# Performance work log

Measured on AMD Instinct MI355X. Metric: run time of the kernel, lower is better.

## Reference

```python
import jax, jax.numpy as jnp
import numpy as np

S, W, H = 1025, 128, 200


def setup_inputs() -> dict:
    key = jax.random.key(0)
    ks = jax.random.split(key, 40)
    n = lambda k, shape, s=1.0: jax.random.normal(k, shape, dtype=jnp.float32) * s
    p = {}
    p["words"] = n(ks[0], (S, W, H))
    p["lengths"] = jax.random.randint(ks[1], (S,), 1, W + 1, dtype=jnp.int32)
    p["h0w"] = n(ks[2], (S, H))
    p["c0w"] = n(ks[3], (S, H))
    p["h0p"] = n(ks[4], (H,))
    p["c0p"] = n(ks[5], (H,))
    p["h0q"] = n(ks[6], (H,))
    p["c0q"] = n(ks[7], (H,))
    ki = 8
    for nm in ("ctx", "tgt", "prev", "post"):
        p[f"wih_{nm}"] = n(ks[ki], (4 * H, H), 0.05); ki += 1
        p[f"whh_{nm}"] = n(ks[ki], (4 * H, H), 0.05); ki += 1
        p[f"bih_{nm}"] = n(ks[ki], (4 * H,), 0.05); ki += 1
        p[f"bhh_{nm}"] = n(ks[ki], (4 * H,), 0.05); ki += 1
    p["fc_w"] = n(ks[ki], (H, 2 * H), 0.05); ki += 1
    p["fc_b"] = n(ks[ki], (H,), 0.05)
    return p


def _lstm_seq(x, h0, c0, wih, whh, bih, bhh):
    """x: [T,H]; returns outputs [T,H]. Torch LSTM gate order: i,f,g,o."""
    gx = x @ wih.T + (bih + bhh)  # precompute input projection: [T,4H]
    def step(carry, g):
        h, c = carry
        gates = g + h @ whh.T
        i, f, gg, o = jnp.split(gates, 4, axis=-1)
        c = jax.nn.sigmoid(f) * c + jax.nn.sigmoid(i) * jnp.tanh(gg)
        h = jax.nn.sigmoid(o) * jnp.tanh(c)
        return (h, c), h
    _, hs = jax.lax.scan(step, (h0, c0), gx)
    return hs


def reference(words, lengths, h0w, c0w, h0p, c0p, h0q, c0q,
              wih_ctx, whh_ctx, bih_ctx, bhh_ctx,
              wih_tgt, whh_tgt, bih_tgt, bhh_tgt,
              wih_prev, whh_prev, bih_prev, bhh_prev,
              wih_post, whh_post, bih_post, bhh_post,
              fc_w, fc_b):
    Sn = words.shape[0]
    mid = (Sn - 1) // 2
    # Word-level context RNN over all sentences (batched scan)
    ctx_outs = jax.vmap(_lstm_seq, in_axes=(0, 0, 0, None, None, None, None))(
        words, h0w, c0w, wih_ctx, whh_ctx, bih_ctx, bhh_ctx)  # [S,W,H]
    # sentence embedding = output at last real word (ragged lengths)
    emb = ctx_outs[jnp.arange(Sn), lengths - 1]  # [S,H]
    # middle sentence uses target RNN instead
    tgt_outs = _lstm_seq(words[mid], h0w[mid], c0w[mid], wih_tgt, whh_tgt, bih_tgt, bhh_tgt)
    emb = emb.at[mid].set(tgt_outs[lengths[mid] - 1])
    # prev RNN over sentences 0..mid; keep output at mid
    prev_hs = _lstm_seq(emb[:mid + 1], h0p, c0p, wih_prev, whh_prev, bih_prev, bhh_prev)
    prev_out = prev_hs[-1]
    # post RNN over sentences S-1..mid (reversed); keep output at mid
    post_hs = _lstm_seq(emb[mid:][::-1], h0q, c0q, wih_post, whh_post, bih_post, bhh_post)
    post_out = post_hs[-1]
    feat = jnp.concatenate([prev_out, post_out])  # [2H]
    return feat @ fc_w.T + fc_b  # [H]
```

## Files before the change

kernel.cpp:

```cpp
#include <hip/hip_runtime.h>
#include <cmath>

typedef unsigned short u16;
typedef short bf16x8 __attribute__((ext_vector_type(8)));
typedef float f32x4 __attribute__((ext_vector_type(4)));

#define S_N 1025
#define W_N 128
#define H_N 200
#define FH_N 800
#define KP 232
#define SGP 911
#define SGW 804
#define MID 512
#define NT 56
#define PKT (NT * 7 * 512)
#define PKC 544
#define QKS 136
#define FRAGSZ (7 * PKC)

__device__ __forceinline__ float bf2f(u16 u) {
  unsigned int x = ((unsigned int)u) << 16;
  return __builtin_bit_cast(float, x);
}
__device__ __forceinline__ u16 f2bf(float f) {
  unsigned int x = __builtin_bit_cast(unsigned int, f);
  x += 0x7fffu + ((x >> 16) & 1u);
  return (u16)(x >> 16);
}
#define LOG2E 1.44269504088896f
__device__ __forceinline__ float fsigm(float x) {
  float e = __builtin_amdgcn_exp2f(-fabsf(x) * LOG2E);
  float p = __builtin_amdgcn_rcpf(1.f + e);
  return x >= 0.f ? p : 1.f - p;
}
__device__ __forceinline__ float ftanh(float x) {
  float e = __builtin_amdgcn_exp2f(-2.f * fabsf(x) * LOG2E);
  float th = (1.f - e) * __builtin_amdgcn_rcpf(1.f + e);
  return x >= 0.f ? th : -th;
}

__device__ __forceinline__ const bf16x8* pkptr(const u16* pk, int tt, int kcc, int lane) {
  return (const bf16x8*)(pk + (size_t)((tt * 7 + kcc) * 512 + lane * 8));
}
__device__ __forceinline__ int fidx(int m, int k) {
  return (k >> 5) * PKC + ((k >> 3) & 3) * QKS + m * 8 + (k & 7);
}
__device__ __forceinline__ const bf16x8* frg(const u16* base, int kcc, int lane) {
  return (const bf16x8*)(base + kcc * PKC + (lane >> 4) * QKS + (lane & 15) * 8);
}

__global__ __launch_bounds__(256) void k_w2b(
    const float* __restrict__ p0, const float* __restrict__ p1,
    const float* __restrict__ p2, const float* __restrict__ p3,
    const float* __restrict__ p4, const float* __restrict__ p5,
    const float* __restrict__ p6, const float* __restrict__ p7,
    u16* __restrict__ dst)
{
  int i = blockIdx.x * 256 + threadIdx.x;
  if (i >= 8 * PKT) return;
  int w = i / PKT, r = i - w * PKT;
  int tt = r / 3584;
  int q = r - tt * 3584;
  int kcc = q >> 9;
  int lane = (q >> 3) & 63;
  int j = q & 7;
  int col = lane & 15, quad = lane >> 4;
  int gate = tt * 16 + col;
  int k = kcc * 32 + quad * 8 + j;
  const float* ps[8] = {p0, p1, p2, p3, p4, p5, p6, p7};
  u16 v = 0;
  if (gate < FH_N && k < H_N) v = f2bf(ps[w][(size_t)gate * H_N + k]);
  dst[i] = v;
}

__global__ __launch_bounds__(1024) void k_sort(
    const int* __restrict__ lengths, int* __restrict__ order)
{
  __shared__ int key[2048], val[2048];
  int tid = threadIdx.x;
  for (int v = 0; v < 2; ++v) {
    int i = tid + v * 1024;
    key[i] = (i < S_N) ? lengths[i] : -1;
    val[i] = (i < S_N) ? i : (S_N - 1);
  }
  __syncthreads();
  for (int k = 2; k <= 2048; k <<= 1)
    for (int j = k >> 1; j > 0; j >>= 1) {
      for (int v = 0; v < 2; ++v) {
        int i = tid + v * 1024;
        int ix = i ^ j;
        if (ix > i) {
          bool descRegion = ((i & k) == 0);
          int ki = key[i], kx = key[ix];
          if ((ki < kx) == descRegion) {
            key[i] = kx; key[ix] = ki;
            int tv = val[i]; val[i] = val[ix]; val[ix] = tv;
          }
        }
      }
      __syncthreads();
    }
  for (int v = 0; v < 2; ++v) {
    int i = tid + v * 1024;
    if (i < S_N) order[i] = val[i];
  }
}

__global__ __launch_bounds__(512, 1) void k_xpack(
    int c, int CH,
    const float* __restrict__ words, const int* __restrict__ lengths,
    const u16* __restrict__ wihb_ctx, const float* __restrict__ bih_ctx, const float* __restrict__ bhh_ctx,
    const u16* __restrict__ wihb_tgt, const float* __restrict__ bih_tgt, const float* __restrict__ bhh_tgt,
    float* __restrict__ gxc)
{
  const int slot = blockIdx.x % 1026;
  const int tile = blockIdx.x / 1026;
  const int t0f = tile * 16;
  const bool tg = (slot == 1025);
  const int s = tg ? MID : slot;
  const int len = lengths[s];
  const int tbase = c * CH + t0f;
  if (t0f >= CH || tbase >= len) return;
  const u16* wih = tg ? wihb_tgt : wihb_ctx;
  const float* bih = tg ? bih_tgt : bih_ctx;
  const float* bhh = tg ? bhh_tgt : bhh_ctx;

  __shared__ __align__(16) u16 sXh[FRAGSZ];
  __shared__ __align__(16) u16 sXl[FRAGSZ];
  __shared__ float sBias[FH_N];
  const int tid = threadIdx.x;
  for (int e = tid; e < FRAGSZ; e += 512) { sXh[e] = 0; sXl[e] = 0; }
  for (int e = tid; e < FH_N; e += 512) sBias[e] = bih[e] + bhh[e];
  __syncthreads();
  const int nrow = min(16, min(CH - t0f, len - tbase));
  for (int e = tid; e < nrow * H_N; e += 512) {
    int tr = e / H_N, k = e - tr * H_N;
    float v = words[((size_t)s * W_N + tbase + tr) * H_N + k];
    u16 vh = f2bf(v);
    int idx = fidx(tr, k);
    sXh[idx] = vh;
    sXl[idx] = f2bf(v - bf2f(vh));
  }
  __syncthreads();

  const int lane = tid & 63, wv = tid >> 6, quad = lane >> 4, col = lane & 15;
  const int tcg = t0f + col;
  const bool okcol = (tcg < CH) && (c * CH + tcg < len);

#pragma unroll
  for (int i = 0; i < 7; ++i) {
    int tt = wv + 8 * i;
    if (tt < 50) {
      f32x4 acc = {0.f, 0.f, 0.f, 0.f};
#pragma unroll
      for (int kcc = 0; kcc < 7; ++kcc) {
        bf16x8 Aw = *pkptr(wih, tt, kcc, lane);
        bf16x8 bxh = *frg(sXh, kcc, lane);
        bf16x8 bxl = *frg(sXl, kcc, lane);
        acc = __builtin_amdgcn_mfma_f32_16x16x32_bf16(Aw, bxh, acc, 0, 0, 0);
        acc = __builtin_amdgcn_mfma_f32_16x16x32_bf16(Aw, bxl, acc, 0, 0, 0);
      }
      if (okcol) {
        float b0 = sBias[tt * 16 + quad * 4 + 0];
        float b1 = sBias[tt * 16 + quad * 4 + 1];
        float b2 = sBias[tt * 16 + quad * 4 + 2];
        float b3 = sBias[tt * 16 + quad * 4 + 3];
        f32x4 o = {acc[0] + b0, acc[1] + b1, acc[2] + b2, acc[3] + b3};
        *(f32x4*)(gxc + ((size_t)slot * CH + tcg) * FH_N + tt * 16 + quad * 4) = o;
      }
    }
  }
}

__global__ __launch_bounds__(512, 1) void k_wrec(
    int c, int CH,
    const int* __restrict__ lengths, const int* __restrict__ order,
    const float* __restrict__ h0w, const float* __restrict__ c0w,
    const u16* __restrict__ whhb_ctx, const u16* __restrict__ whhb_tgt,
    const float* __restrict__ gxc,
    float* __restrict__ stateH, float* __restrict__ stateC,
    float* __restrict__ emb)
{
  const int tid = threadIdx.x;
  const int b = blockIdx.x;
  const bool is_tgt = (b == 65);
  const u16* whh = is_tgt ? whhb_tgt : whhb_ctx;

  __shared__ __align__(16) u16 sBh[FRAGSZ];
  __shared__ __align__(16) u16 sBl[FRAGSZ];
  __shared__ float sG[16 * SGW];
  __shared__ int sLen[16], sId[16];

  if (tid < 16) {
    int slot = b * 16 + tid;
    int s = is_tgt ? MID : order[min(slot, S_N - 1)];
    sId[tid] = s;
    sLen[tid] = lengths[s];
  }
  __syncthreads();
  int Lmax = 1;
  for (int m = 0; m < 16; ++m) Lmax = max(Lmax, sLen[m]);
  if (c * CH >= Lmax) return;

  const int lane = tid & 63;
  const int wv = tid >> 6;
  const int quad = lane >> 4;
  const int col = lane & 15;

  bf16x8 afr[7][7];
#pragma unroll
  for (int i = 0; i < 7; ++i)
#pragma unroll
    for (int kcc = 0; kcc < 7; ++kcc)
      afr[i][kcc] = *pkptr(whh, wv + 8 * i, kcc, lane);

  for (int e = tid; e < FRAGSZ; e += 512) { sBh[e] = 0; sBl[e] = 0; }
  __syncthreads();

  float creg[7];
#pragma unroll
  for (int rr = 0; rr < 7; ++rr) {
    int e = tid + 512 * rr;
    if (e < 16 * H_N) {
      int m = e / H_N, j = e - m * H_N;
      float h, cc;
      if (c == 0) {
        int s = sId[m];
        h = h0w[(size_t)s * H_N + j];
        cc = c0w[(size_t)s * H_N + j];
      } else {
        h = stateH[(size_t)(b * 16 + m) * H_N + j];
        cc = stateC[(size_t)(b * 16 + m) * H_N + j];
      }
      creg[rr] = cc;
      u16 hh = f2bf(h);
      int idx = fidx(m, j);
      sBh[idx] = hh;
      sBl[idx] = f2bf(h - bf2f(hh));
    }
  }
  __syncthreads();

#pragma unroll 1
  for (int tc = 0; tc < CH; ++tc) {
    const int t = c * CH + tc;
    if (t >= Lmax) break;

    f32x4 acc[7];
#pragma unroll
    for (int i = 0; i < 7; ++i) { f32x4 z = {0.f, 0.f, 0.f, 0.f}; acc[i] = z; }
#pragma unroll
    for (int kcc = 0; kcc < 7; ++kcc) {
      bf16x8 bh = *frg(sBh, kcc, lane);
      bf16x8 bl = *frg(sBl, kcc, lane);
#pragma unroll
      for (int i = 0; i < 7; ++i) {
        if (wv + 8 * i < 50) {
          acc[i] = __builtin_amdgcn_mfma_f32_16x16x32_bf16(afr[i][kcc], bh, acc[i], 0, 0, 0);
          acc[i] = __builtin_amdgcn_mfma_f32_16x16x32_bf16(afr[i][kcc], bl, acc[i], 0, 0, 0);
        }
      }
    }
#pragma unroll
    for (int i = 0; i < 7; ++i) {
      int tt = wv + 8 * i;
      if (tt < 50)
        *(f32x4*)(sG + col * SGW + tt * 16 + quad * 4) = acc[i];
    }

    float gv[7][4];
#pragma unroll
    for (int rr = 0; rr < 7; ++rr) {
      int e = tid + 512 * rr;
      if (e < 16 * H_N) {
        int m = e / H_N, j = e - m * H_N;
        int gslot = is_tgt ? 1025 : sId[m];
        const float* gp = gxc + ((size_t)gslot * CH + tc) * FH_N + j;
        gv[rr][0] = gp[0];
        gv[rr][1] = gp[H_N];
        gv[rr][2] = gp[2 * H_N];
        gv[rr][3] = gp[3 * H_N];
      }
    }
    __syncthreads();

#pragma unroll
    for (int rr = 0; rr < 7; ++rr) {
      int e = tid + 512 * rr;
      if (e < 16 * H_N) {
        int m = e / H_N, j = e - m * H_N;
        const float* gRow = sG + m * SGW + j;
        float ig = gRow[0] + gv[rr][0];
        float fg = gRow[H_N] + gv[rr][1];
        float gg = gRow[2 * H_N] + gv[rr][2];
        float og = gRow[3 * H_N] + gv[rr][3];
        float nc = fsigm(fg) * creg[rr] + fsigm(ig) * ftanh(gg);
        float nh = fsigm(og) * ftanh(nc);
        creg[rr] = nc;
        u16 hh = f2bf(nh);
        int idx = fidx(m, j);
        sBh[idx] = hh;
        sBl[idx] = f2bf(nh - bf2f(hh));
        if (t == sLen[m] - 1) {
          int s = sId[m];
          if (is_tgt) {
            if (m == 0) emb[(size_t)MID * H_N + j] = nh;
          } else if (s != MID) {
            emb[(size_t)s * H_N + j] = nh;
          }
        }
      }
    }
    __syncthreads();
  }

#pragma unroll
  for (int rr = 0; rr < 7; ++rr) {
    int e = tid + 512 * rr;
    if (e < 16 * H_N) {
      int m = e / H_N, j = e - m * H_N;
      int idx = fidx(m, j);
      stateH[(size_t)(b * 16 + m) * H_N + j] = bf2f(sBh[idx]) + bf2f(sBl[idx]);
      stateC[(size_t)(b * 16 + m) * H_N + j] = creg[rr];
    }
  }
}

__global__ __launch_bounds__(512, 1) void k_word_s(
    const float* __restrict__ words, const int* __restrict__ lengths,
    const int* __restrict__ order,
    const float* __restrict__ h0w, const float* __restrict__ c0w,
    const u16* __restrict__ wihb_ctx, const u16* __restrict__ whhb_ctx,
    const float* __restrict__ bih_ctx, const float* __restrict__ bhh_ctx,
    const u16* __restrict__ wihb_tgt, const u16* __restrict__ whhb_tgt,
    const float* __restrict__ bih_tgt, const float* __restrict__ bhh_tgt,
    float* __restrict__ emb)
{
  const int tid = threadIdx.x;
  const int b = blockIdx.x;
  const bool is_tgt = (b == 65);
  const u16* wih = is_tgt ? wihb_tgt : wihb_ctx;
  const u16* whh = is_tgt ? whhb_tgt : whhb_ctx;
  const float* bih = is_tgt ? bih_tgt : bih_ctx;
  const float* bhh = is_tgt ? bhh_tgt : bhh_ctx;

  __shared__ __align__(16) u16 sXhi[16 * KP];
  __shared__ __align__(16) u16 sXlo[16 * KP];
  __shared__ __align__(16) u16 sHi[16 * KP];
  __shared__ __align__(16) u16 sLo[16 * KP];
  __shared__ float sG[8 * SGP];
  __shared__ float sB[4 * H_N];
  __shared__ int sLen[16], sId[16];

  for (int e = tid; e < 16 * KP; e += 512) {
    sXhi[e] = 0; sXlo[e] = 0; sHi[e] = 0; sLo[e] = 0;
  }
  if (tid < 16) {
    int slot = b * 16 + tid;
    int s = is_tgt ? MID : order[min(slot, S_N - 1)];
    sId[tid] = s;
    sLen[tid] = lengths[s];
  }
  for (int e = tid; e < 4 * H_N; e += 512) sB[e] = bih[e] + bhh[e];
  __syncthreads();

  float creg[7];
#pragma unroll
  for (int r = 0; r < 7; ++r) {
    int e = tid + 512 * r;
    if (e < 16 * H_N) {
      int m = e / H_N, j = e - m * H_N;
      int s = sId[m];
      float h = h0w[(size_t)s * H_N + j];
      u16 hh = f2bf(h);
      sHi[m * KP + j] = hh;
      sLo[m * KP + j] = f2bf(h - bf2f(hh));
      creg[r] = c0w[(size_t)s * H_N + j];
    }
  }
  __syncthreads();
  int Lmax = 1;
  for (int m = 0; m < 16; ++m) Lmax = max(Lmax, sLen[m]);

  const int lane = tid & 63;
  const int wv = tid >> 6;
  const int quad = lane >> 4;
  const int col = lane & 15;
  const int hpass = quad >> 1;

  const u16* aXh = sXhi + col * KP + quad * 8;
  const u16* aXl = sXlo + col * KP + quad * 8;
  const u16* aHh = sHi  + col * KP + quad * 8;
  const u16* aHl = sLo  + col * KP + quad * 8;

#pragma unroll 1
  for (int t = 0; t < Lmax; ++t) {
    for (int e = tid; e < 16 * H_N; e += 512) {
      int m = e / H_N, k = e - m * H_N;
      float v = words[((size_t)sId[m] * W_N + t) * H_N + k];
      u16 vh = f2bf(v);
      sXhi[m * KP + k] = vh;
      sXlo[m * KP + k] = f2bf(v - bf2f(vh));
    }
    __syncthreads();

    f32x4 acc[7];
#pragma unroll
    for (int i = 0; i < 7; ++i) { f32x4 z4 = {0.f, 0.f, 0.f, 0.f}; acc[i] = z4; }

#pragma unroll
    for (int kcc = 0; kcc < 7; ++kcc) {
      bf16x8 axh = *(const bf16x8*)(aXh + kcc * 32);
      bf16x8 axl = *(const bf16x8*)(aXl + kcc * 32);
      bf16x8 ahh = *(const bf16x8*)(aHh + kcc * 32);
      bf16x8 ahl = *(const bf16x8*)(aHl + kcc * 32);
#pragma unroll
      for (int i = 0; i < 7; ++i) {
        if (wv + 8 * i < 50) {
          bf16x8 bw = *pkptr(wih, wv + 8 * i, kcc, lane);
          bf16x8 bh = *pkptr(whh, wv + 8 * i, kcc, lane);
          acc[i] = __builtin_amdgcn_mfma_f32_16x16x32_bf16(axh, bw, acc[i], 0, 0, 0);
          acc[i] = __builtin_amdgcn_mfma_f32_16x16x32_bf16(axl, bw, acc[i], 0, 0, 0);
          acc[i] = __builtin_amdgcn_mfma_f32_16x16x32_bf16(ahh, bh, acc[i], 0, 0, 0);
          acc[i] = __builtin_amdgcn_mfma_f32_16x16x32_bf16(ahl, bh, acc[i], 0, 0, 0);
        }
      }
    }

#pragma unroll 1
    for (int h = 0; h < 2; ++h) {
      if (hpass == h) {
#pragma unroll
        for (int i = 0; i < 7; ++i) {
          int tt = wv + 8 * i;
          if (tt < 50) {
#pragma unroll
            for (int r = 0; r < 4; ++r)
              sG[((quad & 1) * 4 + r) * SGP + tt * 16 + col] = acc[i][r];
          }
        }
      }
      __syncthreads();
#pragma unroll
      for (int rr = 0; rr < 7; ++rr) {
        int e = tid + 512 * rr;
        if (e < 16 * H_N) {
          int m = e / H_N, j = e - m * H_N;
          if ((m >> 3) == h) {
            const float* gRow = sG + (m - 8 * h) * SGP;
            float ig = gRow[j] + sB[j];
            float fg = gRow[H_N + j] + sB[H_N + j];
            float gg = gRow[2 * H_N + j] + sB[2 * H_N + j];
            float og = gRow[3 * H_N + j] + sB[3 * H_N + j];
            float nc = fsigm(fg) * creg[rr] + fsigm(ig) * ftanh(gg);
            float nh = fsigm(og) * ftanh(nc);
            creg[rr] = nc;
            u16 hh = f2bf(nh);
            sHi[m * KP + j] = hh;
            sLo[m * KP + j] = f2bf(nh - bf2f(hh));
            if (t == sLen[m] - 1) {
              int s = sId[m];
              if (is_tgt) {
                if (m == 0) emb[(size_t)MID * H_N + j] = nh;
              } else if (s != MID) {
                emb[(size_t)s * H_N + j] = nh;
              }
            }
          }
        }
      }
      __syncthreads();
    }
  }
}

__global__ __launch_bounds__(512) void k_gx(
    const float* __restrict__ emb,
    const u16* __restrict__ wihb_prev, const float* __restrict__ bih_prev, const float* __restrict__ bhh_prev,
    const u16* __restrict__ wihb_post, const float* __restrict__ bih_post, const float* __restrict__ bhh_post,
    float* __restrict__ gxp, float* __restrict__ gxq)
{
  const int tid = threadIdx.x;
  const int b = blockIdx.x;
  const bool post = (b >= 33);
  const int t0 = (post ? b - 33 : b) * 16;
  const u16* wih = post ? wihb_post : wihb_prev;
  const float* bih = post ? bih_post : bih_prev;
  const float* bhh = post ? bhh_post : bhh_prev;
  float* out = post ? gxq : gxp;

  __shared__ __align__(16) u16 sEhi[16 * KP];
  __shared__ __align__(16) u16 sElo[16 * KP];
  for (int e = tid; e < 16 * KP; e += 512) { sEhi[e] = 0; sElo[e] = 0; }
  __syncthreads();
  for (int e = tid; e < 16 * H_N; e += 512) {
    int m = e / H_N, k = e - m * H_N;
    int t = t0 + m;
    if (t <= 512) {
      int src = post ? (1024 - t) : t;
      float v = emb[(size_t)src * H_N + k];
      u16 vh = f2bf(v);
      sEhi[m * KP + k] = vh;
      sElo[m * KP + k] = f2bf(v - bf2f(vh));
    }
  }
  __syncthreads();

  const int lane = tid & 63;
  const int wv = tid >> 6;
  const int quad = lane >> 4;
  const int col = lane & 15;
  const u16* aH = sEhi + col * KP + quad * 8;
  const u16* aL = sElo + col * KP + quad * 8;

#pragma unroll 1
  for (int i = 0; i < 7; ++i) {
    int tt = wv + 8 * i;
    if (tt >= 50) break;
    int gate = tt * 16 + col;
    f32x4 acc = {0.f, 0.f, 0.f, 0.f};
#pragma unroll
    for (int kcc = 0; kcc < 7; ++kcc) {
      bf16x8 Ah = *(const bf16x8*)(aH + kcc * 32);
      bf16x8 Al = *(const bf16x8*)(aL + kcc * 32);
      bf16x8 bw = *pkptr(wih, tt, kcc, lane);
      acc = __builtin_amdgcn_mfma_f32_16x16x32_bf16(Ah, bw, acc, 0, 0, 0);
      acc = __builtin_amdgcn_mfma_f32_16x16x32_bf16(Al, bw, acc, 0, 0, 0);
    }
    float bias = bih[gate] + bhh[gate];
#pragma unroll
    for (int r = 0; r < 4; ++r) {
      int t = t0 + quad * 4 + r;
      if (t <= 512) out[(size_t)t * FH_N + gate] = acc[r] + bias;
    }
  }
}

__global__ __launch_bounds__(512, 1) void k_sent(
    const u16* __restrict__ whhb_prev, const u16* __restrict__ whhb_post,
    const float* __restrict__ h0p, const float* __restrict__ c0p,
    const float* __restrict__ h0q, const float* __restrict__ c0q,
    const float* __restrict__ gxp, const float* __restrict__ gxq,
    float* __restrict__ outp, float* __restrict__ outq)
{
  const int tid = threadIdx.x;
  const bool post = (blockIdx.x != 0);
  const u16* whh = post ? whhb_post : whhb_prev;
  const float* h0 = post ? h0q : h0p;
  const float* c0 = post ? c0q : c0p;
  const float* gx = post ? gxq : gxp;
  float* outv = post ? outq : outp;

  __shared__ __align__(16) u16 sHi[224];
  __shared__ __align__(16) u16 sLo[224];
  __shared__ float sGa[FH_N];
  __shared__ float sGb[FH_N];

  const int lane = tid & 63;
  const int wv = tid >> 6;
  const int quad = lane >> 4;
  const int col = lane & 15;

  bf16x8 afr[7][7];
#pragma unroll
  for (int i = 0; i < 7; ++i)
#pragma unroll
    for (int kcc = 0; kcc < 7; ++kcc)
      afr[i][kcc] = *pkptr(whh, wv + 8 * i, kcc, lane);

  if (tid < 224) { sHi[tid] = 0; sLo[tid] = 0; }
  float c = 0.f, last_h = 0.f;
  if (tid < H_N) {
    float h = h0[tid];
    u16 hh = f2bf(h);
    sHi[tid] = hh;
    sLo[tid] = f2bf(h - bf2f(hh));
    c = c0[tid];
  }
  __syncthreads();

  const u16* hb = ((lane & 8) ? sLo : sHi) + quad * 8;
  const bool wrA = (col == 0), wrB = (col == 8);

  float gc0 = 0.f, gc1 = 0.f, gc2 = 0.f, gc3 = 0.f;
  if (tid < H_N) {
    gc0 = gx[tid]; gc1 = gx[H_N + tid]; gc2 = gx[2 * H_N + tid]; gc3 = gx[3 * H_N + tid];
  }

#pragma unroll 1
  for (int t = 0; t < 513; ++t) {
    bf16x8 bfr[7];
#pragma unroll
    for (int kcc = 0; kcc < 7; ++kcc) bfr[kcc] = *(const bf16x8*)(hb + kcc * 32);

    float gn0 = 0.f, gn1 = 0.f, gn2 = 0.f, gn3 = 0.f;
    if (t + 1 < 513 && tid < H_N) {
      const float* g = gx + (size_t)(t + 1) * FH_N;
      gn0 = g[tid]; gn1 = g[H_N + tid]; gn2 = g[2 * H_N + tid]; gn3 = g[3 * H_N + tid];
    }

#pragma unroll
    for (int i = 0; i < 7; ++i) {
      int tt = wv + 8 * i;
      if (tt < 50) {
        f32x4 acc = {0.f, 0.f, 0.f, 0.f};
#pragma unroll
        for (int kcc = 0; kcc < 7; ++kcc)
          acc = __builtin_amdgcn_mfma_f32_16x16x32_bf16(afr[i][kcc], bfr[kcc], acc, 0, 0, 0);
        if (wrA) {
#pragma unroll
          for (int r = 0; r < 4; ++r) sGa[tt * 16 + quad * 4 + r] = acc[r];
        } else if (wrB) {
#pragma unroll
          for (int r = 0; r < 4; ++r) sGb[tt * 16 + quad * 4 + r] = acc[r];
        }
      }
    }
    __syncthreads();

    if (tid < H_N) {
      float ig = sGa[tid] + sGb[tid] + gc0;
      float fg = sGa[H_N + tid] + sGb[H_N + tid] + gc1;
      float gg = sGa[2 * H_N + tid] + sGb[2 * H_N + tid] + gc2;
      float og = sGa[3 * H_N + tid] + sGb[3 * H_N + tid] + gc3;
      float nc = fsigm(fg) * c + fsigm(ig) * ftanh(gg);
      float nh = fsigm(og) * ftanh(nc);
      c = nc;
      last_h = nh;
      u16 hh = f2bf(nh);
      sHi[tid] = hh;
      sLo[tid] = f2bf(nh - bf2f(hh));
    }
    gc0 = gn0; gc1 = gn1; gc2 = gn2; gc3 = gn3;
    __syncthreads();
  }
  if (tid < H_N) outv[tid] = last_h;
}

__global__ __launch_bounds__(256) void k_fc(
    const float* __restrict__ pout, const float* __restrict__ qout,
    const float* __restrict__ fc_w, const float* __restrict__ fc_b,
    float* __restrict__ out)
{
  const int tid = threadIdx.x;
  if (tid < H_N) {
    float d = fc_b[tid];
    const float* wr = fc_w + (size_t)tid * 2 * H_N;
    for (int k = 0; k < H_N; ++k) d += pout[k] * wr[k];
    for (int k = 0; k < H_N; ++k) d += qout[k] * wr[H_N + k];
    out[tid] = d;
  }
}

extern "C" void kernel_launch(void* const* d_in, const int* in_sizes, int n_in,
                              void* d_out, int out_size, void* d_ws, size_t ws_size,
                              hipStream_t stream) {
  const float* words   = (const float*)d_in[0];
  const int*   lengths = (const int*)d_in[1];
  const float* h0w = (const float*)d_in[2];
  const float* c0w = (const float*)d_in[3];
  const float* h0p = (const float*)d_in[4];
  const float* c0p = (const float*)d_in[5];
  const float* h0q = (const float*)d_in[6];
  const float* c0q = (const float*)d_in[7];
  const float* wih_ctx = (const float*)d_in[8];
  const float* whh_ctx = (const float*)d_in[9];
  const float* bih_ctx = (const float*)d_in[10];
  const float* bhh_ctx = (const float*)d_in[11];
  const float* wih_tgt = (const float*)d_in[12];
  const float* whh_tgt = (const float*)d_in[13];
  const float* bih_tgt = (const float*)d_in[14];
  const float* bhh_tgt = (const float*)d_in[15];
  const float* wih_prev = (const float*)d_in[16];
  const float* whh_prev = (const float*)d_in[17];
  const float* bih_prev = (const float*)d_in[18];
  const float* bhh_prev = (const float*)d_in[19];
  const float* wih_post = (const float*)d_in[20];
  const float* whh_post = (const float*)d_in[21];
  const float* bih_post = (const float*)d_in[22];
  const float* bhh_post = (const float*)d_in[23];
  const float* fc_w = (const float*)d_in[24];
  const float* fc_b = (const float*)d_in[25];
  (void)in_sizes; (void)n_in; (void)out_size;

  const size_t FIXF = 1448600;
  int CH = 0;
  for (int cand = 32; cand >= 1; cand >>= 1) {
    size_t needB = ((size_t)1026 * cand * 800 + FIXF) * 4 + 1056 * 4 + (size_t)8 * PKT * 2 + 256;
    if (ws_size >= needB) { CH = cand; break; }
  }

  float* ws = (float*)d_ws;
  float *gxc, *stateH, *stateC, *emb, *gxp, *gxq, *po, *qo;
  int* order;
  u16* wb;
  if (CH > 0) {
    gxc = ws;
    stateH = gxc + (size_t)1026 * CH * 800;
    stateC = stateH + 211200;
    emb = stateC + 211200;
    gxp = emb + 205000;
    gxq = gxp + 410400;
    po = gxq + 410400;
    qo = po + 200;
    order = (int*)(qo + 200);
    wb = (u16*)(order + 1056);
  } else {
    gxc = nullptr; stateH = nullptr; stateC = nullptr;
    emb = ws;
    gxp = ws + 205000;
    gxq = ws + 615400;
    po = ws + 1025800;
    qo = ws + 1026000;
    order = (int*)(ws + 1026200);
    wb = (u16*)(ws + 1027232);
  }
  u16* wihb_ctx  = wb;
  u16* whhb_ctx  = wb + PKT;
  u16* wihb_tgt  = wb + 2 * PKT;
  u16* whhb_tgt  = wb + 3 * PKT;
  u16* whhb_prev = wb + 4 * PKT;
  u16* whhb_post = wb + 5 * PKT;
  u16* wihb_prev = wb + 6 * PKT;
  u16* wihb_post = wb + 7 * PKT;

  k_w2b<<<(8 * PKT + 255) / 256, 256, 0, stream>>>(
      wih_ctx, whh_ctx, wih_tgt, whh_tgt, whh_prev, whh_post,
      wih_prev, wih_post, wb);
  k_sort<<<1, 1024, 0, stream>>>(lengths, order);

  if (CH > 0) {
    const int TT = (CH + 15) / 16;
    const int NC = (W_N + CH - 1) / CH;
    for (int c = 0; c < NC; ++c) {
      k_xpack<<<1026 * TT, 512, 0, stream>>>(c, CH, words, lengths,
                                             wihb_ctx, bih_ctx, bhh_ctx,
                                             wihb_tgt, bih_tgt, bhh_tgt, gxc);
      k_wrec<<<66, 512, 0, stream>>>(c, CH, lengths, order, h0w, c0w,
                                     whhb_ctx, whhb_tgt, gxc, stateH, stateC, emb);
    }
  } else {
    k_word_s<<<66, 512, 0, stream>>>(words, lengths, order, h0w, c0w,
                                     wihb_ctx, whhb_ctx, bih_ctx, bhh_ctx,
                                     wihb_tgt, whhb_tgt, bih_tgt, bhh_tgt, emb);
  }
  k_gx<<<66, 512, 0, stream>>>(emb, wihb_prev, bih_prev, bhh_prev,
                               wihb_post, bih_post, bhh_post, gxp, gxq);
  k_sent<<<2, 512, 0, stream>>>(whhb_prev, whhb_post, h0p, c0p, h0q, c0q,
                                gxp, gxq, po, qo);
  k_fc<<<1, 256, 0, stream>>>(po, qo, fc_w, fc_b, (float*)d_out);
}
```

Baseline: 2.144 ms.

## Interleave gate rows for sentence LSTM and halve k_sent block size

```diff
diff --git a/kernel.cpp b/kernel.cpp
--- a/kernel.cpp
+++ b/kernel.cpp
@@ -66,11 +66,17 @@
   int lane = (q >> 3) & 63;
   int j = q & 7;
   int col = lane & 15, quad = lane >> 4;
-  int gate = tt * 16 + col;
   int k = kcc * 32 + quad * 8 + j;
   const float* ps[8] = {p0, p1, p2, p3, p4, p5, p6, p7};
   u16 v = 0;
-  if (gate < FH_N && k < H_N) v = f2bf(ps[w][(size_t)gate * H_N + k]);
+  if (w == 4 || w == 5) {
+    int jj = tt * 4 + (col >> 2);
+    int gp = col & 3;
+    if (jj < H_N && k < H_N) v = f2bf(ps[w][((size_t)gp * H_N + jj) * H_N + k]);
+  } else {
+    int gate = tt * 16 + col;
+    if (gate < FH_N && k < H_N) v = f2bf(ps[w][(size_t)gate * H_N + k]);
+  }
   dst[i] = v;
 }
 
@@ -529,15 +535,17 @@
       acc = __builtin_amdgcn_mfma_f32_16x16x32_bf16(Al, bw, acc, 0, 0, 0);
     }
     float bias = bih[gate] + bhh[gate];
+    int gp = gate >= 600 ? 3 : (gate >= 400 ? 2 : (gate >= 200 ? 1 : 0));
+    int jg = gate - gp * 200;
 #pragma unroll
     for (int r = 0; r < 4; ++r) {
       int t = t0 + quad * 4 + r;
-      if (t <= 512) out[(size_t)t * FH_N + gate] = acc[r] + bias;
-    }
-  }
-}
-
-__global__ __launch_bounds__(512, 1) void k_sent(
+      if (t <= 512) out[(size_t)t * FH_N + jg * 4 + gp] = acc[r] + bias;
+    }
+  }
+}
+
+__global__ __launch_bounds__(256, 1) void k_sent(
     const u16* __restrict__ whhb_prev, const u16* __restrict__ whhb_post,
     const float* __restrict__ h0p, const float* __restrict__ c0p,
     const float* __restrict__ h0q, const float* __restrict__ c0q,
@@ -554,20 +562,19 @@
 
   __shared__ __align__(16) u16 sHi[224];
   __shared__ __align__(16) u16 sLo[224];
-  __shared__ float sGa[FH_N];
-  __shared__ float sGb[FH_N];
+  __shared__ __align__(16) float sGt[H_N * 8];
 
   const int lane = tid & 63;
   const int wv = tid >> 6;
   const int quad = lane >> 4;
   const int col = lane & 15;
 
-  bf16x8 afr[7][7];
-#pragma unroll
-  for (int i = 0; i < 7; ++i)
+  bf16x8 afr[13][7];
+#pragma unroll
+  for (int i = 0; i < 13; ++i)
 #pragma unroll
     for (int kcc = 0; kcc < 7; ++kcc)
-      afr[i][kcc] = *pkptr(whh, wv + 8 * i, kcc, lane);
+      afr[i][kcc] = *pkptr(whh, wv + 4 * i, kcc, lane);
 
   if (tid < 224) { sHi[tid] = 0; sLo[tid] = 0; }
   float c = 0.f, last_h = 0.f;
@@ -581,12 +588,11 @@
   __syncthreads();
 
   const u16* hb = ((lane & 8) ? sLo : sHi) + quad * 8;
-  const bool wrA = (col == 0), wrB = (col == 8);
-
-  float gc0 = 0.f, gc1 = 0.f, gc2 = 0.f, gc3 = 0.f;
-  if (tid < H_N) {
-    gc0 = gx[tid]; gc1 = gx[H_N + tid]; gc2 = gx[2 * H_N + tid]; gc3 = gx[3 * H_N + tid];
-  }
+  const bool wr = ((col & 7) == 0);
+  const int wroff = (col >> 1);
+
+  f32x4 gc = {0.f, 0.f, 0.f, 0.f};
+  if (tid < H_N) gc = *(const f32x4*)(gx + (size_t)tid * 4);
 
 #pragma unroll 1
   for (int t = 0; t < 513; ++t) {
@@ -594,36 +600,45 @@
 #pragma unroll
     for (int kcc = 0; kcc < 7; ++kcc) bfr[kcc] = *(const bf16x8*)(hb + kcc * 32);
 
-    float gn0 = 0.f, gn1 = 0.f, gn2 = 0.f, gn3 = 0.f;
-    if (t + 1 < 513 && tid < H_N) {
-      const float* g = gx + (size_t)(t + 1) * FH_N;
-      gn0 = g[tid]; gn1 = g[H_N + tid]; gn2 = g[2 * H_N + tid]; gn3 = g[3 * H_N + tid];
-    }
-
-#pragma unroll
-    for (int i = 0; i < 7; ++i) {
-      int tt = wv + 8 * i;
-      if (tt < 50) {
-        f32x4 acc = {0.f, 0.f, 0.f, 0.f};
-#pragma unroll
-        for (int kcc = 0; kcc < 7; ++kcc)
-          acc = __builtin_amdgcn_mfma_f32_16x16x32_bf16(afr[i][kcc], bfr[kcc], acc, 0, 0, 0);
-        if (wrA) {
-#pragma unroll
-          for (int r = 0; r < 4; ++r) sGa[tt * 16 + quad * 4 + r] = acc[r];
-        } else if (wrB) {
-#pragma unroll
-          for (int r = 0; r < 4; ++r) sGb[tt * 16 + quad * 4 + r] = acc[r];
-        }
+    f32x4 gn = {0.f, 0.f, 0.f, 0.f};
+    if (t + 1 < 513 && tid < H_N)
+      gn = *(const f32x4*)(gx + (size_t)(t + 1) * FH_N + tid * 4);
+
+#pragma unroll
+    for (int g0 = 0; g0 < 2; ++g0) {
+      const int nacc = g0 ? 6 : 7;
+      f32x4 acc[7];
+#pragma unroll
+      for (int i = 0; i < 7; ++i) { f32x4 z = {0.f, 0.f, 0.f, 0.f}; acc[i] = z; }
+#pragma unroll
+      for (int kcc = 0; kcc < 7; ++kcc)
+#pragma unroll
+        for (int i = 0; i < 7; ++i)
+          if (i < nacc) {
+            int tt = wv + 4 * (g0 * 7 + i);
+            if (tt < 50)
+              acc[i] = __builtin_amdgcn_mfma_f32_16x16x32_bf16(
+                  afr[g0 * 7 + i][kcc], bfr[kcc], acc[i], 0, 0, 0);
+          }
+      if (wr) {
+#pragma unroll
+        for (int i = 0; i < 7; ++i)
+          if (i < nacc) {
+            int tt = wv + 4 * (g0 * 7 + i);
+            if (tt < 50)
+              *(f32x4*)(sGt + (tt * 4 + quad) * 8 + wroff) = acc[i];
+          }
       }
     }
     __syncthreads();
 
     if (tid < H_N) {
-      float ig = sGa[tid] + sGb[tid] + gc0;
-      float fg = sGa[H_N + tid] + sGb[H_N + tid] + gc1;
-      float gg = sGa[2 * H_N + tid] + sGb[2 * H_N + tid] + gc2;
-      float og = sGa[3 * H_N + tid] + sGb[3 * H_N + tid] + gc3;
+      f32x4 ga = *(const f32x4*)(sGt + tid * 8);
+      f32x4 gb = *(const f32x4*)(sGt + tid * 8 + 4);
+      float ig = ga[0] + gb[0] + gc[0];
+      float fg = ga[1] + gb[1] + gc[1];
+      float gg = ga[2] + gb[2] + gc[2];
+      float og = ga[3] + gb[3] + gc[3];
       float nc = fsigm(fg) * c + fsigm(ig) * ftanh(gg);
       float nh = fsigm(og) * ftanh(nc);
       c = nc;
@@ -632,7 +647,7 @@
       sHi[tid] = hh;
       sLo[tid] = f2bf(nh - bf2f(hh));
     }
-    gc0 = gn0; gc1 = gn1; gc2 = gn2; gc3 = gn3;
+    gc = gn;
     __syncthreads();
   }
   if (tid < H_N) outv[tid] = last_h;
@@ -747,7 +762,7 @@
   }
   k_gx<<<66, 512, 0, stream>>>(emb, wihb_prev, bih_prev, bhh_prev,
                                wihb_post, bih_post, bhh_post, gxp, gxq);
-  k_sent<<<2, 512, 0, stream>>>(whhb_prev, whhb_post, h0p, c0p, h0q, c0q,
+  k_sent<<<2, 256, 0, stream>>>(whhb_prev, whhb_post, h0p, c0p, h0q, c0q,
                                 gxp, gxq, po, qo);
   k_fc<<<1, 256, 0, stream>>>(po, qo, fc_w, fc_b, (float*)d_out);
 }
```

Measured after the change: 2.696 ms. 25.8% more time.
